# Performance work log

Measured on AMD Instinct MI355X. Metric: run time of the kernel, lower is better.

## Reference

```python
import jax, jax.numpy as jnp
import numpy as np
import math

KERNEL_SIZE = 3
D_MODEL = 1024
D_K = 64
N_HEADS = 16
B = 512
L = 60  # hardcoded by the 60x60 att_sig Gaussian mask in the original module
LN_EPS = 1e-5


def _make_att_sig():
    # Faithful to the torch __init__: Gaussian bump per row, then the
    # (quirky) broadcast normalization att_sig * (1/att_sig.sum(1)),
    # which scales COLUMN j by 1/rowsum_j due to numpy/torch broadcasting.
    x = np.arange(L, dtype=np.float64)
    sig = math.sqrt(KERNEL_SIZE)
    rows = [np.exp(-(x - u) ** 2 / (2 * sig ** 2)) / (math.sqrt(2 * math.pi) * sig) for u in range(L)]
    a = np.stack(rows, axis=0).astype(np.float32)
    a = a * (1.0 / a.sum(1))  # broadcasts over last axis, as in the original
    return jnp.asarray(a)


def _layernorm(h, w, b):
    m = jnp.mean(h, axis=-1, keepdims=True)
    v = jnp.var(h, axis=-1, keepdims=True)
    return (h - m) * jax.lax.rsqrt(v + LN_EPS) * w + b


def setup_inputs() -> dict:
    key = jax.random.key(0)
    ks = jax.random.split(key, 8)
    s_in = 1.0 / math.sqrt(D_MODEL)
    s_ff = 1.0 / math.sqrt(2 * D_MODEL)
    return {
        "x": jax.random.normal(ks[0], (B, L, D_MODEL), jnp.float32),
        "att_sig": _make_att_sig(),
        "wq": jax.random.normal(ks[1], (N_HEADS * D_K, D_MODEL), jnp.float32) * s_in,
        "wk": jax.random.normal(ks[2], (N_HEADS * D_K, D_MODEL), jnp.float32) * s_in,
        "wv": jax.random.normal(ks[3], (N_HEADS * D_K, D_MODEL), jnp.float32) * s_in,
        "wo": jax.random.normal(ks[4], (D_MODEL, N_HEADS * D_K), jnp.float32) * s_in,
        "ln1_w": jnp.ones((D_MODEL,), jnp.float32),
        "ln1_b": jnp.zeros((D_MODEL,), jnp.float32),
        "ffn_w1": jax.random.normal(ks[5], (2 * D_MODEL, D_MODEL), jnp.float32) * s_in,
        "ffn_w2": jax.random.normal(ks[6], (D_MODEL, 2 * D_MODEL), jnp.float32) * s_ff,
        "ln2_w": jnp.ones((D_MODEL,), jnp.float32),
        "ln2_b": jnp.zeros((D_MODEL,), jnp.float32),
    }


def reference(x, att_sig, wq, wk, wv, wo, ln1_w, ln1_b, ffn_w1, ffn_w2, ln2_w, ln2_b):
    b, l, c = x.shape
    # QKV projections -> [B, H, L, d_k]
    q = (x @ wq.T).reshape(b, l, N_HEADS, D_K).transpose(0, 2, 1, 3)
    k = (x @ wk.T).reshape(b, l, N_HEADS, D_K).transpose(0, 2, 1, 3)
    v = (x @ wv.T).reshape(b, l, N_HEADS, D_K).transpose(0, 2, 1, 3)
    scores = jnp.einsum('bhqd,bhkd->bhqk', q, k) / math.sqrt(D_K)
    attn = jax.nn.softmax(scores, axis=-1)  # [B, H, L, L]
    diff = attn - att_sig[None, None]
    loss = jnp.sum(diff * diff)
    ctx = jnp.einsum('bhqk,bhkd->bhqd', attn, v)
    ctx = ctx.transpose(0, 2, 1, 3).reshape(b, l, N_HEADS * D_K)
    out = _layernorm(ctx @ wo.T + x, ln1_w, ln1_b)
    ff = jax.nn.relu(out @ ffn_w1.T) @ ffn_w2.T
    out2 = _layernorm(ff + out, ln2_w, ln2_b)
    return out2, loss
```

## Files before the change

kernel.cpp:

```cpp
#include <hip/hip_runtime.h>
#include <hip/hip_bf16.h>
#include <cstdint>

#define DM   1024
#define DFF  2048
#define NH   16
#define DK   64
#define BBATCH 512
#define LSEQ 60
#define M_TOK (BBATCH*LSEQ)
#define NQKV (3*DM)
#define NTM  120

typedef __attribute__((ext_vector_type(8))) short bf16x8;
typedef __attribute__((ext_vector_type(4))) float f32x4;
typedef __attribute__((ext_vector_type(8))) unsigned short u16x8;
typedef __attribute__((ext_vector_type(4))) unsigned short u16x4;

__device__ __forceinline__ unsigned short f2bf(float f) {
  union { float f; unsigned u; } x; x.f = f;
  unsigned r = x.u + 0x7fffu + ((x.u >> 16) & 1u);
  return (unsigned short)(r >> 16);
}

__device__ __forceinline__ void gload_lds16(const void* g, void* l) {
  __builtin_amdgcn_global_load_lds(
      (const __attribute__((address_space(1))) unsigned int*)g,
      (__attribute__((address_space(3))) unsigned int*)l, 16, 0, 0);
}

template<int MO,int NO>
__device__ __forceinline__ void mf8(f32x4 (&acc)[8][4], const bf16x8 (&a)[4][2],
                                    const bf16x8 (&b)[2][2]) {
#pragma unroll
  for (int m=0;m<4;++m)
#pragma unroll
    for (int n=0;n<2;++n)
#pragma unroll
      for (int ks=0;ks<2;++ks)
        acc[MO+m][NO+n] = __builtin_amdgcn_mfma_f32_16x16x32_bf16(a[m][ks], b[n][ks], acc[MO+m][NO+n], 0,0,0);
}

#define A0S 0
#define A1S 16384
#define B0S 32768
#define B1S 49152

template<int MODE>
__global__ __launch_bounds__(512, 2)
void gemm256(const unsigned short* __restrict__ A, int lda,
             const unsigned short* __restrict__ B, int ldb,
             void* __restrict__ Cv, int ldc,
             const float* __restrict__ Res, int K) {
  __shared__ unsigned short sm[65536];
  const int t  = threadIdx.x;
  const int l  = t & 63, w = t >> 6;
  const int lo = l & 15, hi = l >> 4;
  const int wr = w >> 2, wc = w & 3;
  const int swz = (lo & 7) << 4;

  const int nwg = (int)gridDim.x;
  int wg = (int)blockIdx.x;
  wg = (wg & 7) * (nwg >> 3) + (wg >> 3);
  const int ng  = wg / (NTM*4);
  const int rem = wg - ng*(NTM*4);
  const long row0 = (long)(rem >> 2) * 256;
  const long col0 = (long)(ng*4 + (rem & 3)) * 256;

  const int srow = w*16 + (l>>3);
  const int scol = ((l & 7) ^ (l >> 3)) * 8;
  const unsigned short* pa = A + (size_t)(row0 + srow)*lda + scol;
  const unsigned short* pb = B + (size_t)(col0 + srow)*ldb + scol;
  const size_t ldaj = (size_t)8*lda,  ldah = (size_t)128*lda;
  const size_t ldbj = (size_t)8*ldb,  ldbh = (size_t)128*ldb;
  const int dls = (w*2)*512;

#define STAGE_A(bufS, h, kt) do { \
    const unsigned short* _s = pa + (size_t)(h)*ldah + (size_t)(kt)*64; \
    gload_lds16(_s,        &sm[(bufS) + (h)*8192 + dls]); \
    gload_lds16(_s + ldaj, &sm[(bufS) + (h)*8192 + dls + 512]); \
  } while(0)
#define STAGE_B(bufS, h, kt) do { \
    const unsigned short* _s = pb + (size_t)(h)*ldbh + (size_t)(kt)*64; \
    gload_lds16(_s,        &sm[(bufS) + (h)*8192 + dls]); \
    gload_lds16(_s + ldbj, &sm[(bufS) + (h)*8192 + dls + 512]); \
  } while(0)
#define LDA8(dst, bufS, mbase) do { \
  _Pragma("unroll") for (int m=0;m<4;++m) \
  _Pragma("unroll") for (int ks=0;ks<2;++ks) \
    dst[m][ks] = *(const bf16x8*)((const char*)sm + (bufS)*2 + \
        (wr*128 + ((mbase)+m)*16 + lo)*128 + ((ks*64 + hi*16) ^ swz)); \
  } while(0)
#define LDB4(dst, bufS, nbase) do { \
  _Pragma("unroll") for (int n=0;n<2;++n) \
  _Pragma("unroll") for (int ks=0;ks<2;++ks) \
    dst[n][ks] = *(const bf16x8*)((const char*)sm + (bufS)*2 + \
        (wc*64 + ((nbase)+n)*16 + lo)*128 + ((ks*64 + hi*16) ^ swz)); \
  } while(0)
#define BAR __builtin_amdgcn_s_barrier()
#define LG0 asm volatile("s_waitcnt lgkmcnt(0)" ::: "memory")
#define LG8 asm volatile("s_waitcnt lgkmcnt(8)" ::: "memory")
#define P1S __builtin_amdgcn_s_setprio(1)
#define P0S __builtin_amdgcn_s_setprio(0)

  f32x4 acc[8][4];
#pragma unroll
  for (int m=0;m<8;++m)
#pragma unroll
    for (int n=0;n<4;++n) acc[m][n] = (f32x4){0.f,0.f,0.f,0.f};

  const int nkt = K >> 6;

  STAGE_A(A0S, 0, 0); STAGE_A(A0S, 1, 0);
  STAGE_B(B0S, 0, 0); STAGE_B(B0S, 1, 0);
  STAGE_A(A1S, 0, 1); STAGE_A(A1S, 1, 1);
  STAGE_B(B1S, 0, 1); STAGE_B(B1S, 1, 1);
  asm volatile("s_waitcnt vmcnt(8)" ::: "memory");
  BAR;

  for (int kt = 0; kt + 2 < nkt; kt += 2) {
    bf16x8 a[4][2], b0[2][2], b2[2][2];
    LDA8(a, A0S, 0); LDB4(b0, B0S, 0);
    LG8; BAR; LG0;
    P1S; mf8<0,0>(acc, a, b0); P0S; BAR;
    LDB4(b2, B0S, 2);
    BAR; LG0;
    P1S; mf8<0,2>(acc, a, b2); P0S; BAR;
    LDA8(a, A0S, 4);
    STAGE_B(B0S, 0, kt+2);
    BAR; LG0;
    P1S; mf8<4,0>(acc, a, b0); P0S; BAR;
    STAGE_B(B0S, 1, kt+2);
    asm volatile("s_waitcnt vmcnt(4)" ::: "memory");
    BAR;
    P1S; mf8<4,2>(acc, a, b2); P0S; BAR;
    LDA8(a, A1S, 0); LDB4(b0, B1S, 0);
    STAGE_A(A0S, 0, kt+2);
    LG8; BAR; LG0;
    P1S; mf8<0,0>(acc, a, b0); P0S; BAR;
    LDB4(b2, B1S, 2);
    STAGE_A(A0S, 1, kt+2);
    BAR; LG0;
    P1S; mf8<0,2>(acc, a, b2); P0S; BAR;
    LDA8(a, A1S, 4);
    STAGE_B(B1S, 0, kt+3); STAGE_B(B1S, 1, kt+3);
    BAR; LG0;
    P1S; mf8<4,0>(acc, a, b0); P0S; BAR;
    STAGE_A(A1S, 0, kt+3); STAGE_A(A1S, 1, kt+3);
    asm volatile("s_waitcnt vmcnt(8)" ::: "memory");
    BAR;
    P1S; mf8<4,2>(acc, a, b2); P0S; BAR;
  }

  {
    bf16x8 a[4][2], b0[2][2], b2[2][2];
    LDA8(a, A0S, 0); LDB4(b0, B0S, 0);
    LG8; BAR; LG0; P1S; mf8<0,0>(acc, a, b0); P0S; BAR;
    LDB4(b2, B0S, 2);
    BAR; LG0; P1S; mf8<0,2>(acc, a, b2); P0S; BAR;
    LDA8(a, A0S, 4);
    BAR; LG0; P1S; mf8<4,0>(acc, a, b0); P0S; BAR;
    asm volatile("s_waitcnt vmcnt(0)" ::: "memory");
    BAR; P1S; mf8<4,2>(acc, a, b2); P0S; BAR;
    LDA8(a, A1S, 0); LDB4(b0, B1S, 0);
    LG8; BAR; LG0; P1S; mf8<0,0>(acc, a, b0); P0S; BAR;
    LDB4(b2, B1S, 2);
    BAR; LG0; P1S; mf8<0,2>(acc, a, b2); P0S; BAR;
    LDA8(a, A1S, 4);
    BAR; LG0; P1S; mf8<4,0>(acc, a, b0); P0S; BAR;
    P1S; mf8<4,2>(acc, a, b2); P0S;
  }

#pragma unroll
  for (int m=0;m<8;++m) {
#pragma unroll
    for (int r=0;r<4;++r) {
      const long row = row0 + wr*128 + m*16 + hi*4 + r;
      const size_t base = (size_t)row * ldc;
#pragma unroll
      for (int n=0;n<4;++n) {
        const long col = col0 + wc*64 + n*16 + lo;
        const float v = acc[m][n][r];
        if (MODE == 0) {
          ((unsigned short*)Cv)[base + col] = f2bf(v);
        } else if (MODE == 1) {
          ((float*)Cv)[base + col] = v + Res[base + col];
        } else {
          ((unsigned short*)Cv)[base + col] = f2bf(v > 0.f ? v : 0.f);
        }
      }
    }
  }
#undef STAGE_A
#undef STAGE_B
#undef LDA8
#undef LDB4
#undef BAR
#undef LG0
#undef LG8
#undef P1S
#undef P0S
}

__global__ __launch_bounds__(256)
void attn_kernel(unsigned short* qkv, const float* __restrict__ att_sig,
                 float* __restrict__ loss_part) {
  __shared__ unsigned short qs[64*64], ks[64*64], vts[64*64], as2[64*64];
  __shared__ float red[4];
  const int bid = blockIdx.x;
  const int b = bid >> 4, h = bid & 15;
  const int t = threadIdx.x;
  const int l = t & 63, w = t >> 6, lo = l & 15, hi = l >> 4;

#pragma unroll
  for (int p=0;p<2;++p) {
    int row = p*32 + (t>>3);
    int d0  = (t&7)*8;
    u16x8 zq = {0,0,0,0,0,0,0,0}; u16x8 zk = zq; u16x8 zv = zq;
    if (row < LSEQ) {
      size_t g = (size_t)(b*LSEQ + row)*NQKV + h*DK + d0;
      zq = *(const u16x8*)(qkv + g);
      zk = *(const u16x8*)(qkv + g + DM);
      zv = *(const u16x8*)(qkv + g + 2*DM);
    }
    *(u16x8*)&qs[row*64 + d0] = zq;
    *(u16x8*)&ks[row*64 + d0] = zk;
#pragma unroll
    for (int j=0;j<8;++j) vts[(d0+j)*64 + row] = zv[j];
  }
  __syncthreads();

  f32x4 zero4 = {0.f,0.f,0.f,0.f};
  f32x4 sacc[4];
#pragma unroll
  for (int ct=0;ct<4;++ct) sacc[ct] = zero4;
  bf16x8 aq[2];
  aq[0] = *(const bf16x8*)&qs[(w*16+lo)*64 + hi*8];
  aq[1] = *(const bf16x8*)&qs[(w*16+lo)*64 + 32 + hi*8];
#pragma unroll
  for (int ct=0;ct<4;++ct)
#pragma unroll
    for (int kk=0;kk<2;++kk) {
      bf16x8 bk = *(const bf16x8*)&ks[(ct*16+lo)*64 + kk*32 + hi*8];
      sacc[ct] = __builtin_amdgcn_mfma_f32_16x16x32_bf16(aq[kk], bk, sacc[ct], 0,0,0);
    }

  float lloss = 0.f;
  const float SC = 0.125f;
#pragma unroll
  for (int r=0;r<4;++r) {
    int row = w*16 + hi*4 + r;
    float v0 = sacc[0][r]*SC, v1 = sacc[1][r]*SC, v2 = sacc[2][r]*SC;
    float v3 = (lo < 12) ? sacc[3][r]*SC : -__builtin_inff();
    float mx = fmaxf(fmaxf(v0,v1), fmaxf(v2,v3));
#pragma unroll
    for (int d=1; d<16; d<<=1) mx = fmaxf(mx, __shfl_xor(mx, d, 64));
    float p0=__expf(v0-mx), p1=__expf(v1-mx), p2=__expf(v2-mx), p3=__expf(v3-mx);
    float sm = p0+p1+p2+p3;
#pragma unroll
    for (int d=1; d<16; d<<=1) sm += __shfl_xor(sm, d, 64);
    float inv = 1.0f / sm;
    float a0=p0*inv, a1=p1*inv, a2=p2*inv, a3=p3*inv;
    if (row < LSEQ) {
      float df;
      df = a0 - att_sig[row*LSEQ + lo];       lloss += df*df;
      df = a1 - att_sig[row*LSEQ + 16 + lo];  lloss += df*df;
      df = a2 - att_sig[row*LSEQ + 32 + lo];  lloss += df*df;
      if (lo < 12) { df = a3 - att_sig[row*LSEQ + 48 + lo]; lloss += df*df; }
    }
    as2[row*64 + lo]      = f2bf(a0);
    as2[row*64 + 16 + lo] = f2bf(a1);
    as2[row*64 + 32 + lo] = f2bf(a2);
    as2[row*64 + 48 + lo] = f2bf(a3);
  }
  __syncthreads();

  f32x4 cacc[4];
#pragma unroll
  for (int n=0;n<4;++n) cacc[n] = zero4;
  bf16x8 ap[2];
  ap[0] = *(const bf16x8*)&as2[(w*16+lo)*64 + hi*8];
  ap[1] = *(const bf16x8*)&as2[(w*16+lo)*64 + 32 + hi*8];
#pragma unroll
  for (int n=0;n<4;++n)
#pragma unroll
    for (int kk=0;kk<2;++kk) {
      bf16x8 bv = *(const bf16x8*)&vts[(n*16+lo)*64 + kk*32 + hi*8];
      cacc[n] = __builtin_amdgcn_mfma_f32_16x16x32_bf16(ap[kk], bv, cacc[n], 0,0,0);
    }
#pragma unroll
  for (int r=0;r<4;++r) {
    int row = w*16 + hi*4 + r;
    if (row < LSEQ) {
      size_t g = (size_t)(b*LSEQ + row)*NQKV + h*DK;
#pragma unroll
      for (int n=0;n<4;++n)
        qkv[g + n*16 + lo] = f2bf(cacc[n][r]);
    }
  }

#pragma unroll
  for (int d=1; d<64; d<<=1) lloss += __shfl_xor(lloss, d, 64);
  if (l == 0) red[w] = lloss;
  __syncthreads();
  if (t == 0) loss_part[bid] = red[0]+red[1]+red[2]+red[3];
}

__global__ __launch_bounds__(256)
void reduce_loss(const float* __restrict__ part, float* __restrict__ out) {
  __shared__ float red[4];
  float s = 0.f;
  for (int i = threadIdx.x; i < BBATCH*NH; i += 256) s += part[i];
#pragma unroll
  for (int d=1; d<64; d<<=1) s += __shfl_xor(s, d, 64);
  if ((threadIdx.x & 63) == 0) red[threadIdx.x >> 6] = s;
  __syncthreads();
  if (threadIdx.x == 0) out[0] = red[0]+red[1]+red[2]+red[3];
}

template<int WB>
__global__ __launch_bounds__(256)
void ln_kernel(float* __restrict__ io, const float* __restrict__ gw,
               const float* __restrict__ gb, unsigned short* __restrict__ ob) {
  __shared__ float red[4];
  const int t = threadIdx.x;
  const size_t base = (size_t)blockIdx.x * DM;
  float4 v = ((const float4*)(io + base))[t];
  float s = v.x+v.y+v.z+v.w;
#pragma unroll
  for (int d=1; d<64; d<<=1) s += __shfl_xor(s, d, 64);
  if ((t&63)==0) red[t>>6] = s;
  __syncthreads();
  float mean = (red[0]+red[1]+red[2]+red[3]) * (1.f/DM);
  __syncthreads();
  float dx0=v.x-mean, dx1=v.y-mean, dx2=v.z-mean, dx3=v.w-mean;
  float q = dx0*dx0+dx1*dx1+dx2*dx2+dx3*dx3;
#pragma unroll
  for (int d=1; d<64; d<<=1) q += __shfl_xor(q, d, 64);
  if ((t&63)==0) red[t>>6] = q;
  __syncthreads();
  float var = (red[0]+red[1]+red[2]+red[3]) * (1.f/DM);
  float inv = rsqrtf(var + 1e-5f);
  float4 wv = ((const float4*)gw)[t];
  float4 bv = ((const float4*)gb)[t];
  float4 o;
  o.x = dx0*inv*wv.x + bv.x;
  o.y = dx1*inv*wv.y + bv.y;
  o.z = dx2*inv*wv.z + bv.z;
  o.w = dx3*inv*wv.w + bv.w;
  ((float4*)(io + base))[t] = o;
  if (WB) {
    u16x4 ub; ub[0]=f2bf(o.x); ub[1]=f2bf(o.y); ub[2]=f2bf(o.z); ub[3]=f2bf(o.w);
    *(u16x4*)(ob + base + t*4) = ub;
  }
}

__global__ __launch_bounds__(256)
void cast_all(const float* __restrict__ x,  const float* __restrict__ wq,
              const float* __restrict__ wk, const float* __restrict__ wv,
              const float* __restrict__ wo, const float* __restrict__ w1,
              const float* __restrict__ w2,
              unsigned short* __restrict__ xb, unsigned short* __restrict__ wqkvb,
              unsigned short* __restrict__ wob, unsigned short* __restrict__ w1b,
              unsigned short* __restrict__ w2b) {
  const int b = blockIdx.x;
  const float* src; unsigned short* dst; int off;
  if (b < 7680)      { src = x;  dst = xb;              off = b; }
  else if (b < 7936) { src = wq; dst = wqkvb;           off = b - 7680; }
  else if (b < 8192) { src = wk; dst = wqkvb + 1048576; off = b - 7936; }
  else if (b < 8448) { src = wv; dst = wqkvb + 2097152; off = b - 8192; }
  else if (b < 8704) { src = wo; dst = wob;             off = b - 8448; }
  else if (b < 9216) { src = w1; dst = w1b;             off = b - 8704; }
  else               { src = w2; dst = w2b;             off = b - 9216; }
  int i = off*1024 + threadIdx.x;
#pragma unroll
  for (int u=0; u<4; ++u, i += 256) {
    float4 v = ((const float4*)src)[i];
    u16x4 p; p[0]=f2bf(v.x); p[1]=f2bf(v.y); p[2]=f2bf(v.z); p[3]=f2bf(v.w);
    ((u16x4*)dst)[i] = p;
  }
}

extern "C" void kernel_launch(void* const* d_in, const int* in_sizes, int n_in,
                              void* d_out, int out_size, void* d_ws, size_t ws_size,
                              hipStream_t stream) {
  const float* x      = (const float*)d_in[0];
  const float* attsig = (const float*)d_in[1];
  const float* wq     = (const float*)d_in[2];
  const float* wk     = (const float*)d_in[3];
  const float* wv     = (const float*)d_in[4];
  const float* wo     = (const float*)d_in[5];
  const float* ln1w   = (const float*)d_in[6];
  const float* ln1b   = (const float*)d_in[7];
  const float* w1     = (const float*)d_in[8];
  const float* w2     = (const float*)d_in[9];
  const float* ln2w   = (const float*)d_in[10];
  const float* ln2b   = (const float*)d_in[11];

  char* ws = (char*)d_ws;
  unsigned short* xb    = (unsigned short*)(ws);
  unsigned short* wqkvb = (unsigned short*)(ws + 62914560ull);
  unsigned short* wob   = (unsigned short*)(ws + 69206016ull);
  unsigned short* w1b   = (unsigned short*)(ws + 71303168ull);
  unsigned short* w2b   = (unsigned short*)(ws + 75497472ull);
  unsigned short* qkv   = (unsigned short*)(ws + 79691776ull);
  unsigned short* h1    = (unsigned short*)(ws + 268435456ull);
  float*          lpart = (float*)(ws + 394264576ull);

  float* outf = (float*)d_out;
  float* loss = outf + (size_t)M_TOK*DM;

  cast_all<<<9728,256,0,stream>>>(x, wq, wk, wv, wo, w1, w2,
                                  xb, wqkvb, wob, w1b, w2b);

  gemm256<0><<<NTM*(NQKV/256), 512, 0, stream>>>(xb, DM, wqkvb, DM, qkv, NQKV, nullptr, DM);

  attn_kernel<<<BBATCH*NH, 256, 0, stream>>>(qkv, attsig, lpart);
  reduce_loss<<<1,256,0,stream>>>(lpart, loss);

  gemm256<1><<<NTM*(DM/256), 512, 0, stream>>>(qkv, NQKV, wob, DM, outf, DM, x, DM);
  ln_kernel<1><<<M_TOK,256,0,stream>>>(outf, ln1w, ln1b, xb);
  gemm256<2><<<NTM*(DFF/256), 512, 0, stream>>>(xb, DM, w1b, DM, h1, DFF, nullptr, DM);
  gemm256<1><<<NTM*(DM/256), 512, 0, stream>>>(h1, DFF, w2b, DFF, outf, DM, outf, DFF);
  ln_kernel<0><<<M_TOK,256,0,stream>>>(outf, ln2w, ln2b, nullptr);
}
```

Measured before the change: 760.1 us.

## Double-buffer GEMM LDS fragments in registers to overlap reads with MFMA

Restructures the GEMM main loop so LDS reads for the next MFMA sub-block are issued one phase ahead into a second register set (aA/aB, bX/bY). Partial lgkmcnt waits with sched_barrier replace full drains, and the vmcnt waits are retimed. The aim is to hide LDS latency behind matrix-core work. In exchange it uses more VGPRs, which may lower occupancy or cause spills, and the finer-grained wait counts are easy to get wrong and could create races.

```diff
diff --git a/kernel.cpp b/kernel.cpp
--- a/kernel.cpp
+++ b/kernel.cpp
@@ -85,21 +85,22 @@
     gload_lds16(_s,        &sm[(bufS) + (h)*8192 + dls]); \
     gload_lds16(_s + ldbj, &sm[(bufS) + (h)*8192 + dls + 512]); \
   } while(0)
-#define LDA8(dst, bufS, mbase) do { \
+#define RD_A(dst, bufS, mbase) do { \
   _Pragma("unroll") for (int m=0;m<4;++m) \
   _Pragma("unroll") for (int ks=0;ks<2;++ks) \
     dst[m][ks] = *(const bf16x8*)((const char*)sm + (bufS)*2 + \
         (wr*128 + ((mbase)+m)*16 + lo)*128 + ((ks*64 + hi*16) ^ swz)); \
   } while(0)
-#define LDB4(dst, bufS, nbase) do { \
+#define RD_B(dst, bufS, nbase) do { \
   _Pragma("unroll") for (int n=0;n<2;++n) \
   _Pragma("unroll") for (int ks=0;ks<2;++ks) \
     dst[n][ks] = *(const bf16x8*)((const char*)sm + (bufS)*2 + \
         (wc*64 + ((nbase)+n)*16 + lo)*128 + ((ks*64 + hi*16) ^ swz)); \
   } while(0)
 #define BAR __builtin_amdgcn_s_barrier()
-#define LG0 asm volatile("s_waitcnt lgkmcnt(0)" ::: "memory")
-#define LG8 asm volatile("s_waitcnt lgkmcnt(8)" ::: "memory")
+#define LGK(n) do { asm volatile("s_waitcnt lgkmcnt(" #n ")" ::: "memory"); \
+                    __builtin_amdgcn_sched_barrier(0); } while(0)
+#define VMC(n) asm volatile("s_waitcnt vmcnt(" #n ")" ::: "memory")
 #define P1S __builtin_amdgcn_s_setprio(1)
 #define P0S __builtin_amdgcn_s_setprio(0)
 
@@ -110,65 +111,64 @@
     for (int n=0;n<4;++n) acc[m][n] = (f32x4){0.f,0.f,0.f,0.f};
 
   const int nkt = K >> 6;
+  bf16x8 aA[4][2], aB[4][2], bX[2][2], bY[2][2];
 
   STAGE_A(A0S, 0, 0); STAGE_A(A0S, 1, 0);
   STAGE_B(B0S, 0, 0); STAGE_B(B0S, 1, 0);
   STAGE_A(A1S, 0, 1); STAGE_A(A1S, 1, 1);
   STAGE_B(B1S, 0, 1); STAGE_B(B1S, 1, 1);
-  asm volatile("s_waitcnt vmcnt(8)" ::: "memory");
+  VMC(8);
   BAR;
+  RD_A(aA, A0S, 0); RD_B(bX, B0S, 0);
 
   for (int kt = 0; kt + 2 < nkt; kt += 2) {
-    bf16x8 a[4][2], b0[2][2], b2[2][2];
-    LDA8(a, A0S, 0); LDB4(b0, B0S, 0);
-    LG8; BAR; LG0;
-    P1S; mf8<0,0>(acc, a, b0); P0S; BAR;
-    LDB4(b2, B0S, 2);
-    BAR; LG0;
-    P1S; mf8<0,2>(acc, a, b2); P0S; BAR;
-    LDA8(a, A0S, 4);
+    RD_B(bY, B0S, 2);
+    BAR; LGK(4);
+    P1S; mf8<0,0>(acc, aA, bX); P0S; BAR;
+    RD_A(aB, A0S, 4);
+    BAR; LGK(8);
+    P1S; mf8<0,2>(acc, aA, bY); P0S; BAR;
     STAGE_B(B0S, 0, kt+2);
-    BAR; LG0;
-    P1S; mf8<4,0>(acc, a, b0); P0S; BAR;
+    VMC(2);
+    BAR; LGK(0);
+    P1S; mf8<4,0>(acc, aB, bX); P0S; BAR;
+    RD_A(aA, A1S, 0); RD_B(bX, B1S, 0);
     STAGE_B(B0S, 1, kt+2);
-    asm volatile("s_waitcnt vmcnt(4)" ::: "memory");
-    BAR;
-    P1S; mf8<4,2>(acc, a, b2); P0S; BAR;
-    LDA8(a, A1S, 0); LDB4(b0, B1S, 0);
+    BAR; LGK(12);
+    P1S; mf8<4,2>(acc, aB, bY); P0S; BAR;
+    RD_B(bY, B1S, 2);
     STAGE_A(A0S, 0, kt+2);
-    LG8; BAR; LG0;
-    P1S; mf8<0,0>(acc, a, b0); P0S; BAR;
-    LDB4(b2, B1S, 2);
+    BAR; LGK(4);
+    P1S; mf8<0,0>(acc, aA, bX); P0S; BAR;
+    RD_A(aB, A1S, 4);
     STAGE_A(A0S, 1, kt+2);
-    BAR; LG0;
-    P1S; mf8<0,2>(acc, a, b2); P0S; BAR;
-    LDA8(a, A1S, 4);
+    BAR; LGK(8);
+    P1S; mf8<0,2>(acc, aA, bY); P0S; BAR;
     STAGE_B(B1S, 0, kt+3); STAGE_B(B1S, 1, kt+3);
-    BAR; LG0;
-    P1S; mf8<4,0>(acc, a, b0); P0S; BAR;
+    VMC(4);
+    BAR; LGK(0);
+    P1S; mf8<4,0>(acc, aB, bX); P0S; BAR;
+    RD_A(aA, A0S, 0); RD_B(bX, B0S, 0);
     STAGE_A(A1S, 0, kt+3); STAGE_A(A1S, 1, kt+3);
-    asm volatile("s_waitcnt vmcnt(8)" ::: "memory");
-    BAR;
-    P1S; mf8<4,2>(acc, a, b2); P0S; BAR;
+    BAR; LGK(12);
+    P1S; mf8<4,2>(acc, aB, bY); P0S; BAR;
   }
 
   {
-    bf16x8 a[4][2], b0[2][2], b2[2][2];
-    LDA8(a, A0S, 0); LDB4(b0, B0S, 0);
-    LG8; BAR; LG0; P1S; mf8<0,0>(acc, a, b0); P0S; BAR;
-    LDB4(b2, B0S, 2);
-    BAR; LG0; P1S; mf8<0,2>(acc, a, b2); P0S; BAR;
-    LDA8(a, A0S, 4);
-    BAR; LG0; P1S; mf8<4,0>(acc, a, b0); P0S; BAR;
-    asm volatile("s_waitcnt vmcnt(0)" ::: "memory");
-    BAR; P1S; mf8<4,2>(acc, a, b2); P0S; BAR;
-    LDA8(a, A1S, 0); LDB4(b0, B1S, 0);
-    LG8; BAR; LG0; P1S; mf8<0,0>(acc, a, b0); P0S; BAR;
-    LDB4(b2, B1S, 2);
-    BAR; LG0; P1S; mf8<0,2>(acc, a, b2); P0S; BAR;
-    LDA8(a, A1S, 4);
-    BAR; LG0; P1S; mf8<4,0>(acc, a, b0); P0S; BAR;
-    P1S; mf8<4,2>(acc, a, b2); P0S;
+    RD_B(bY, B0S, 2);
+    BAR; LGK(4); P1S; mf8<0,0>(acc, aA, bX); P0S; BAR;
+    RD_A(aB, A0S, 4);
+    BAR; LGK(8); P1S; mf8<0,2>(acc, aA, bY); P0S; BAR;
+    VMC(0);
+    BAR; LGK(0); P1S; mf8<4,0>(acc, aB, bX); P0S; BAR;
+    RD_A(aA, A1S, 0); RD_B(bX, B1S, 0);
+    BAR; LGK(12); P1S; mf8<4,2>(acc, aB, bY); P0S; BAR;
+    RD_B(bY, B1S, 2);
+    BAR; LGK(4); P1S; mf8<0,0>(acc, aA, bX); P0S; BAR;
+    RD_A(aB, A1S, 4);
+    BAR; LGK(8); P1S; mf8<0,2>(acc, aA, bY); P0S; BAR;
+    BAR; LGK(0); P1S; mf8<4,0>(acc, aB, bX); P0S; BAR;
+    LGK(0); P1S; mf8<4,2>(acc, aB, bY); P0S;
   }
 
 #pragma unroll
@@ -193,11 +193,11 @@
   }
 #undef STAGE_A
 #undef STAGE_B
-#undef LDA8
-#undef LDB4
+#undef RD_A
+#undef RD_B
 #undef BAR
-#undef LG0
-#undef LG8
+#undef LGK
+#undef VMC
 #undef P1S
 #undef P0S
 }
```

After: 1.974 ms. 2.6x slower.
